# Kernel tuning notes

Hardware: AMD Instinct MI355X
Metric: run time of the kernel (lower is better)

Reference implementation:

```python
import jax, jax.numpy as jnp
import numpy as np
from jax import lax

B, C, H, W = 32, 512, 14, 14
NA = 9
N = H * W * NA  # 1764 anchors per image
IOU_THR = 0.3
SCORE_THR = 0.5
TOPK = 50


def setup_inputs() -> dict:
    key = jax.random.key(0)
    ks = jax.random.split(key, 8)
    def w(k, shape):
        return jax.random.normal(k, shape, jnp.float32) * 0.01  # nn.init.normal_(std=0.01)
    inp = {"features": jax.random.normal(ks[0], (B, C, H, W), jnp.float32)}
    # bbox head: 512->256 (GN32) ->128 (GN16) ->128 (GN16) -> 4*NA (1x1)
    inp["b1w"] = w(ks[1], (256, 512, 3, 3)); inp["b1b"] = jnp.zeros(256)
    inp["bg1w"] = jnp.ones(256); inp["bg1b"] = jnp.zeros(256)
    inp["b2w"] = w(ks[2], (128, 256, 3, 3)); inp["b2b"] = jnp.zeros(128)
    inp["bg2w"] = jnp.ones(128); inp["bg2b"] = jnp.zeros(128)
    inp["b3w"] = w(ks[3], (128, 128, 3, 3)); inp["b3b"] = jnp.zeros(128)
    inp["bg3w"] = jnp.ones(128); inp["bg3b"] = jnp.zeros(128)
    inp["b4w"] = w(ks[4], (4 * NA, 128, 1, 1)); inp["b4b"] = jnp.zeros(4 * NA)
    # classification head: 512->256 (GN32) ->128 (GN16) -> NA (1x1)
    inp["c1w"] = w(ks[5], (256, 512, 3, 3)); inp["c1b"] = jnp.zeros(256)
    inp["cg1w"] = jnp.ones(256); inp["cg1b"] = jnp.zeros(256)
    inp["c2w"] = w(ks[6], (128, 256, 3, 3)); inp["c2b"] = jnp.zeros(128)
    inp["cg2w"] = jnp.ones(128); inp["cg2b"] = jnp.zeros(128)
    inp["c3w"] = w(ks[7], (NA, 128, 1, 1)); inp["c3b"] = jnp.zeros(NA)
    return inp


def conv(x, w, b):
    k = w.shape[-1]
    pad = ((k // 2, k // 2), (k // 2, k // 2))
    y = lax.conv_general_dilated(x, w, (1, 1), pad, dimension_numbers=("NCHW", "OIHW", "NCHW"))
    return y + b[None, :, None, None]


def group_norm(x, w, b, groups, eps=1e-5):
    Bn, Cn, Hn, Wn = x.shape
    xg = x.reshape(Bn, groups, Cn // groups, Hn, Wn)
    mu = xg.mean(axis=(2, 3, 4), keepdims=True)
    var = xg.var(axis=(2, 3, 4), keepdims=True)
    xg = (xg - mu) * lax.rsqrt(var + eps)
    return xg.reshape(Bn, Cn, Hn, Wn) * w[None, :, None, None] + b[None, :, None, None]


def gelu(x):
    return jax.nn.gelu(x, approximate=False)  # torch nn.GELU default (erf)


def nms_single(boxes, scores):
    # boxes [N,4], scores [N]; greedy NMS, fixed-shape padded output [TOPK,5]
    valid = scores > SCORE_THR
    boxes = jnp.clip(boxes, 0.0, 1.0)
    order = jnp.argsort(-jnp.where(valid, scores, -jnp.inf))  # desc, invalid last
    b = boxes[order]; s = scores[order]; v = valid[order]
    x1 = jnp.maximum(b[:, None, 0], b[None, :, 0])
    y1 = jnp.maximum(b[:, None, 1], b[None, :, 1])
    x2 = jnp.minimum(b[:, None, 2], b[None, :, 2])
    y2 = jnp.minimum(b[:, None, 3], b[None, :, 3])
    inter = jnp.clip(x2 - x1, 0.0) * jnp.clip(y2 - y1, 0.0)
    area = (b[:, 2] - b[:, 0]) * (b[:, 3] - b[:, 1])
    iou = inter / (area[:, None] + area[None, :] - inter)
    # torch keeps when iou < thr; NaN compares False -> suppressed. Replicate exactly:
    suppress = jnp.logical_not(iou < IOU_THR)  # [N,N] bool
    idxs = jnp.arange(N)
    def body(suppressed, xs):
        row, i, vi = xs
        keep_i = vi & jnp.logical_not(suppressed[i])
        return suppressed | (keep_i & row & (idxs > i)), keep_i
    _, keep = lax.scan(body, jnp.zeros(N, bool), (suppress, idxs, v))
    kept_scores = jnp.where(keep, s, -1.0)
    topv, topi = lax.top_k(kept_scores, TOPK)  # first <=50 kept in score order
    out_boxes = jnp.where(topv[:, None] > 0.0, b[topi], 0.0)
    return jnp.concatenate([out_boxes, topv[:, None]], axis=-1)  # [TOPK, 5]; score=-1 marks pad


def _forward(features, b1w, b1b, bg1w, bg1b, b2w, b2b, bg2w, bg2b, b3w, b3b, bg3w, bg3b, b4w, b4b, c1w, c1b, cg1w, cg1b, c2w, c2b, cg2w, cg2b, c3w, c3b):
    bs = features.shape[0]
    h = group_norm(gelu(conv(features, b1w, b1b)), bg1w, bg1b, 32)
    h = group_norm(gelu(conv(h, b2w, b2b)), bg2w, bg2b, 16)
    h = group_norm(gelu(conv(h, b3w, b3b)), bg3w, bg3b, 16)
    bbox = conv(h, b4w, b4b).transpose(0, 2, 3, 1).reshape(bs, -1, 4)  # [B,N,4]
    h = group_norm(gelu(conv(features, c1w, c1b)), cg1w, cg1b, 32)
    h = group_norm(gelu(conv(h, c2w, c2b)), cg2w, cg2b, 16)
    conf = jax.nn.sigmoid(conv(h, c3w, c3b).transpose(0, 2, 3, 1).reshape(bs, -1))  # [B,N]
    return jax.vmap(nms_single)(bbox, conf)  # [B,TOPK,5]


def reference(features, b1w, b1b, bg1w, bg1b, b2w, b2b, bg2w, bg2b, b3w, b3b, bg3w, bg3b, b4w, b4b, c1w, c1b, cg1w, cg1b, c2w, c2b, cg2w, cg2b, c3w, c3b):
    return _forward(features, b1w, b1b, bg1w, bg1b, b2w, b2b, bg2w, bg2b, b3w, b3b, bg3w, bg3b, b4w, b4b, c1w, c1b, cg1w, cg1b, c2w, c2b, cg2w, cg2b, c3w, c3b)
```

## Files before the change

kernel.cpp:

```cpp
#include <hip/hip_runtime.h>
#include <hip/hip_bf16.h>
#include <math.h>

#define CHUNK 16
#define NN 1764
#define SORTN 2048

typedef float v2f __attribute__((ext_vector_type(2)));

template<int Co, int Ci>
__device__ inline void seg_pack_pk(const float* __restrict__ src, float* __restrict__ dst, int i) {
  int co = i / (Ci * 9); int rem = i - co * (Ci * 9); int ci = rem / 9; int k = rem - ci * 9;
  int p = (co >> 5) * 16 + (co & 15);
  int h = (co & 31) >> 4;
  dst[((size_t)ci * (Co >> 1) + p) * 20 + 2 * k + h] = src[i];
}
template<int Co, int CiK>
__device__ inline void seg_tr(const float* __restrict__ src, float* __restrict__ dst, int i) {
  int co = i / CiK; int cik = i - co * CiK;
  dst[cik * Co + co] = src[i];
}

__global__ void wtrans_all(
  const float* __restrict__ b1w, const float* __restrict__ c1w,
  const float* __restrict__ b2w, const float* __restrict__ c2w,
  const float* __restrict__ b3w, const float* __restrict__ b4w,
  const float* __restrict__ c3w,
  float* __restrict__ wp1b, float* __restrict__ wp1c,
  float* __restrict__ wp2b, float* __restrict__ wp2c,
  float* __restrict__ wp3b, float* __restrict__ wt4b, float* __restrict__ wt3c)
{
  int j = blockIdx.x * blockDim.x + threadIdx.x;
  if (j < 1179648) { seg_pack_pk<256, 512>(b1w, wp1b, j); return; } j -= 1179648;
  if (j < 1179648) { seg_pack_pk<256, 512>(c1w, wp1c, j); return; } j -= 1179648;
  if (j < 294912)  { seg_pack_pk<128, 256>(b2w, wp2b, j); return; } j -= 294912;
  if (j < 294912)  { seg_pack_pk<128, 256>(c2w, wp2c, j); return; } j -= 294912;
  if (j < 147456)  { seg_pack_pk<128, 128>(b3w, wp3b, j); return; } j -= 147456;
  if (j < 4608)    { seg_tr<36, 128>(b4w, wt4b, j); return; }  j -= 4608;
  if (j < 1152)    { seg_tr<9, 128>(c3w, wt3c, j); return; }
}

template<int COPT>
__global__ __launch_bounds__(256, 2) void conv3x3_part(
    const float* __restrict__ in0, const float* __restrict__ in1,
    const float* __restrict__ wt0, const float* __restrict__ wt1,
    float* __restrict__ po0, float* __restrict__ po1,
    int Cin, int Cout, int cobPerHead, int cinPerSplit, size_t sStride)
{
  constexpr int NP = COPT / 2;
  const int tid = threadIdx.x;
  const int bx  = blockIdx.x;
  const int b   = blockIdx.y;
  const int s   = blockIdx.z;
  const int head = bx / cobPerHead;
  const int cob  = bx - head * cobPerHead;
  const float* in  = head ? in1  : in0;
  const float* wt  = head ? wt1  : wt0;
  float* po        = head ? po1  : po0;
  const int co0 = cob * (16 * COPT);

  const int col = tid & 15;
  const int r   = tid >> 4;
  const bool ract = r < 14;

  __shared__ float tile[2][CHUNK][16][16];

  {
    float* tz = &tile[0][0][0][0];
    for (int i = tid; i < 2 * CHUNK * 256; i += 256) tz[i] = 0.0f;
  }
  __syncthreads();

  const int p = tid;
  const bool pa = p < 196;
  const int prow = p / 14, pcol = p - prow * 14;
  const float* inb = in + (size_t)b * Cin * 196;
  const int cb0 = (s * cinPerSplit) / CHUNK;
  const int nch = cinPerSplit / CHUNK;
  const int CoutH = Cout >> 1;

  int pidx[NP];
#pragma unroll
  for (int g = 0; g < NP; ++g) pidx[g] = ((co0 >> 5) + g) * 16 + col;

  if (pa) {
#pragma unroll
    for (int ci = 0; ci < CHUNK; ++ci)
      tile[0][ci][prow + 1][pcol + 1] = inb[(cb0 * CHUNK + ci) * 196 + p];
  }
  __syncthreads();

  v2f acc[NP][14];
#pragma unroll
  for (int g = 0; g < NP; ++g)
#pragma unroll
    for (int j = 0; j < 14; ++j) acc[g][j] = (v2f)(0.0f);

  for (int lcb = 0; lcb < nch; ++lcb) {
    const int cbg = cb0 + lcb;
    const int cur = lcb & 1;
    const bool more = (lcb + 1 < nch);
    float v[CHUNK];
    if (more && pa) {
#pragma unroll
      for (int ci = 0; ci < CHUNK; ++ci)
        v[ci] = inb[((cbg + 1) * CHUNK + ci) * 196 + p];
    }
    if (ract) {
      for (int ci = 0; ci < CHUNK; ++ci) {
        v2f w2[NP][9];
#pragma unroll
        for (int g = 0; g < NP; ++g) {
          const float4* wq = (const float4*)(wt +
              ((size_t)(cbg * CHUNK + ci) * CoutH + pidx[g]) * 20);
          float4 q0 = wq[0], q1 = wq[1], q2 = wq[2], q3 = wq[3], q4 = wq[4];
          w2[g][0] = (v2f){q0.x, q0.y}; w2[g][1] = (v2f){q0.z, q0.w};
          w2[g][2] = (v2f){q1.x, q1.y}; w2[g][3] = (v2f){q1.z, q1.w};
          w2[g][4] = (v2f){q2.x, q2.y}; w2[g][5] = (v2f){q2.z, q2.w};
          w2[g][6] = (v2f){q3.x, q3.y}; w2[g][7] = (v2f){q3.z, q3.w};
          w2[g][8] = (v2f){q4.x, q4.y};
        }
        float nb[3][16];
#pragma unroll
        for (int dr = 0; dr < 3; ++dr) {
          const float4* rp = (const float4*)(&tile[cur][ci][r + dr][0]);
          float4 a = rp[0], bq = rp[1], cq = rp[2], dq = rp[3];
          nb[dr][0]  = a.x;  nb[dr][1]  = a.y;  nb[dr][2]  = a.z;  nb[dr][3]  = a.w;
          nb[dr][4]  = bq.x; nb[dr][5]  = bq.y; nb[dr][6]  = bq.z; nb[dr][7]  = bq.w;
          nb[dr][8]  = cq.x; nb[dr][9]  = cq.y; nb[dr][10] = cq.z; nb[dr][11] = cq.w;
          nb[dr][12] = dq.x; nb[dr][13] = dq.y; nb[dr][14] = dq.z; nb[dr][15] = dq.w;
        }
#pragma unroll
        for (int ky = 0; ky < 3; ++ky)
#pragma unroll
          for (int kx = 0; kx < 3; ++kx) {
#pragma unroll
            for (int g = 0; g < NP; ++g) {
              v2f w = w2[g][ky * 3 + kx];
#pragma unroll
              for (int j = 0; j < 14; ++j) {
                float s_ = nb[ky][j + kx];
                v2f nbv = (v2f){s_, s_};
                acc[g][j] = __builtin_elementwise_fma(w, nbv, acc[g][j]);
              }
            }
          }
      }
    }
    if (more && pa) {
#pragma unroll
      for (int ci = 0; ci < CHUNK; ++ci)
        tile[1 - cur][ci][prow + 1][pcol + 1] = v[ci];
    }
    __syncthreads();
  }

  if (ract) {
#pragma unroll
    for (int g = 0; g < NP; ++g) {
      const int ocx = 32 * g + col;
      const int ocy = ocx + 16;
      float* opx = po + (size_t)s * sStride + ((size_t)b * Cout + co0 + ocx) * 196 + r * 14;
      float* opy = po + (size_t)s * sStride + ((size_t)b * Cout + co0 + ocy) * 196 + r * 14;
#pragma unroll
      for (int j = 0; j < 14; ++j) { opx[j] = acc[g][j].x; opy[j] = acc[g][j].y; }
    }
  }
}

template<int S>
__global__ __launch_bounds__(256) void combine_gn(
    const float* __restrict__ po0, const float* __restrict__ po1,
    const float* __restrict__ bs0, const float* __restrict__ bs1,
    const float* __restrict__ gw0, const float* __restrict__ gw1,
    const float* __restrict__ gb0, const float* __restrict__ gb1,
    float* __restrict__ out0, float* __restrict__ out1,
    int Cout, int cobPerHead, size_t sStride)
{
  const int tid = threadIdx.x, bx = blockIdx.x, b = blockIdx.y;
  const int head = bx / cobPerHead, cob = bx - head * cobPerHead;
  const float* po = head ? po1 : po0;
  const float* bs = head ? bs1 : bs0;
  const float* gw = head ? gw1 : gw0;
  const float* gb = head ? gb1 : gb0;
  float* out      = head ? out1 : out0;
  const int co0 = cob * 16;

  __shared__ float red[4][4];
  __shared__ float stats[4];

  const int p = tid;
  const bool pa = p < 196;
  float v[16];
  float s0 = 0.f, q0 = 0.f, s1 = 0.f, q1 = 0.f;
  if (pa) {
#pragma unroll
    for (int c = 0; c < 16; ++c) {
      const size_t base = ((size_t)b * Cout + co0 + c) * 196 + p;
      float x = bs[co0 + c];
#pragma unroll
      for (int s = 0; s < S; ++s) x += po[base + (size_t)s * sStride];
      float g = 0.5f * x * (1.0f + erff(x * 0.70710678118654752440f));
      v[c] = g;
      if (c < 8) { s0 += g; q0 += g * g; } else { s1 += g; q1 += g * g; }
    }
  }
#pragma unroll
  for (int off = 32; off > 0; off >>= 1) {
    s0 += __shfl_down(s0, off, 64); q0 += __shfl_down(q0, off, 64);
    s1 += __shfl_down(s1, off, 64); q1 += __shfl_down(q1, off, 64);
  }
  const int wave = tid >> 6, lane = tid & 63;
  if (lane == 0) { red[wave][0] = s0; red[wave][1] = q0; red[wave][2] = s1; red[wave][3] = q1; }
  __syncthreads();
  if (tid == 0) {
    float S0 = red[0][0] + red[1][0] + red[2][0] + red[3][0];
    float Q0 = red[0][1] + red[1][1] + red[2][1] + red[3][1];
    float S1 = red[0][2] + red[1][2] + red[2][2] + red[3][2];
    float Q1 = red[0][3] + red[1][3] + red[2][3] + red[3][3];
    float m0 = S0 * (1.0f / 1568.0f);
    float v0 = Q0 * (1.0f / 1568.0f) - m0 * m0;
    float m1 = S1 * (1.0f / 1568.0f);
    float v1 = Q1 * (1.0f / 1568.0f) - m1 * m1;
    stats[0] = m0; stats[1] = 1.0f / sqrtf(v0 + 1e-5f);
    stats[2] = m1; stats[3] = 1.0f / sqrtf(v1 + 1e-5f);
  }
  __syncthreads();
  if (pa) {
    float m0 = stats[0], i0 = stats[1], m1 = stats[2], i1 = stats[3];
#pragma unroll
    for (int c = 0; c < 16; ++c) {
      float m  = (c < 8) ? m0 : m1;
      float iv = (c < 8) ? i0 : i1;
      float y = (v[c] - m) * iv * gw[co0 + c] + gb[co0 + c];
      out[((size_t)b * Cout + co0 + c) * 196 + p] = y;
    }
  }
}

__global__ __launch_bounds__(256) void heads_1x1(
    const float* __restrict__ tb, const float* __restrict__ tc,
    const float* __restrict__ wtb, const float* __restrict__ wtc,
    const float* __restrict__ bb,  const float* __restrict__ bc,
    float* __restrict__ bbox, float* __restrict__ conf)
{
  const int b = blockIdx.x, og = blockIdx.y, tid = threadIdx.x;
  if (tid >= 196) return;
  const int p = tid;
  const bool isConf = (og == 4);
  const float* in = isConf ? tc : tb;
  const float* wbase = isConf ? wtc : (wtb + og * 9);
  const int wstride = isConf ? 9 : 36;
  const float* bsrc = isConf ? bc : (bb + og * 9);

  float a[9];
#pragma unroll
  for (int o = 0; o < 9; ++o) a[o] = bsrc[o];
  const float* pin = in + (size_t)b * 128 * 196 + p;
  for (int ci = 0; ci < 128; ++ci) {
    float x = pin[ci * 196];
    const float* w = wbase + ci * wstride;
#pragma unroll
    for (int o = 0; o < 9; ++o) a[o] = fmaf(w[o], x, a[o]);
  }
  if (isConf) {
    float* cf = conf + (size_t)b * NN + (size_t)p * 9;
#pragma unroll
    for (int o = 0; o < 9; ++o) cf[o] = 1.0f / (1.0f + expf(-a[o]));
  } else {
    float* bp = bbox + ((size_t)b * NN) * 4 + (size_t)p * 36 + og * 9;
#pragma unroll
    for (int o = 0; o < 9; ++o) bp[o] = a[o];
  }
}

__global__ __launch_bounds__(512) void nms_kernel(
  const float* __restrict__ bbox, const float* __restrict__ conf, float* __restrict__ out)
{
  const int b = blockIdx.x, tid = threadIdx.x;
  __shared__ unsigned long long key[SORTN];
  __shared__ float sx1[NN], sy1[NN], sx2[NN], sy2[NN], sar[NN], ssc[NN];
  __shared__ unsigned char sup[NN];
  __shared__ int sV, sMin;

  if (tid == 0) sV = 0;
  __syncthreads();
  int cntv = 0;
  const float* cf = conf + (size_t)b * NN;
  for (int i = tid; i < SORTN; i += 512) {
    unsigned long long k;
    if (i < NN) {
      float s = cf[i];
      unsigned rank = (unsigned)(NN - 1 - i);
      if (s > 0.5f) { k = (((unsigned long long)__float_as_uint(s)) << 32) | rank; cntv++; }
      else k = (unsigned long long)rank;
    } else k = 0ull;
    key[i] = k;
  }
  atomicAdd(&sV, cntv);
  __syncthreads();
  const int V = sV;

  for (int kk = 2; kk <= SORTN; kk <<= 1) {
    for (int j = kk >> 1; j > 0; j >>= 1) {
      for (int i = tid; i < SORTN; i += 512) {
        int ixj = i ^ j;
        if (ixj > i) {
          unsigned long long a = key[i], c = key[ixj];
          bool dirDesc = ((i & kk) == 0);
          if ((a < c) == dirDesc) { key[i] = c; key[ixj] = a; }
        }
      }
      __syncthreads();
    }
  }

  const float* bbb = bbox + (size_t)b * NN * 4;
  for (int i = tid; i < V; i += 512) {
    unsigned long long k = key[i];
    int idx = NN - 1 - (int)(unsigned)(k & 0xFFFFFFFFull);
    float s = __uint_as_float((unsigned)(k >> 32));
    const float* bp = bbb + (size_t)idx * 4;
    float x1 = fminf(fmaxf(bp[0], 0.0f), 1.0f);
    float y1 = fminf(fmaxf(bp[1], 0.0f), 1.0f);
    float x2 = fminf(fmaxf(bp[2], 0.0f), 1.0f);
    float y2 = fminf(fmaxf(bp[3], 0.0f), 1.0f);
    sx1[i] = x1; sy1[i] = y1; sx2[i] = x2; sy2[i] = y2;
    sar[i] = (x2 - x1) * (y2 - y1);
    ssc[i] = s;
    sup[i] = 0;
  }
  __syncthreads();

  int kept = 0, cur = 0;
  float* ob = out + (size_t)b * 50 * 5;
  while (kept < 50 && cur < V) {
    int nxt = -1;
    for (int base = cur; base < V; base += 512) {
      if (tid == 0) sMin = 0x7FFFFFFF;
      __syncthreads();
      int i = base + tid;
      if (i < V && !sup[i]) atomicMin(&sMin, i);
      __syncthreads();
      if (sMin != 0x7FFFFFFF) { nxt = sMin; break; }
    }
    if (nxt < 0) break;
    float kx1 = sx1[nxt], ky1 = sy1[nxt], kx2 = sx2[nxt], ky2 = sy2[nxt], ka = sar[nxt];
    if (tid == 0) {
      float* rr = ob + kept * 5;
      rr[0] = kx1; rr[1] = ky1; rr[2] = kx2; rr[3] = ky2; rr[4] = ssc[nxt];
    }
    kept++;
    for (int jj = nxt + 1 + tid; jj < V; jj += 512) {
      if (!sup[jj]) {
        float xx1 = fmaxf(kx1, sx1[jj]);
        float yy1 = fmaxf(ky1, sy1[jj]);
        float xx2 = fminf(kx2, sx2[jj]);
        float yy2 = fminf(ky2, sy2[jj]);
        float inter = fmaxf(xx2 - xx1, 0.0f) * fmaxf(yy2 - yy1, 0.0f);
        float iou = inter / ((ka + sar[jj]) - inter);
        if (!(iou < 0.3f)) sup[jj] = 1;
      }
    }
    cur = nxt + 1;
    __syncthreads();
  }
  for (int rr = kept + tid; rr < 50; rr += 512) {
    float* qq = ob + rr * 5;
    qq[0] = 0.0f; qq[1] = 0.0f; qq[2] = 0.0f; qq[3] = 0.0f; qq[4] = -1.0f;
  }
}

extern "C" void kernel_launch(void* const* d_in, const int* in_sizes, int n_in,
                              void* d_out, int out_size, void* d_ws, size_t ws_size,
                              hipStream_t stream)
{
  const float* features = (const float*)d_in[0];
  const float* b1w = (const float*)d_in[1];  const float* b1b = (const float*)d_in[2];
  const float* bg1w = (const float*)d_in[3]; const float* bg1b = (const float*)d_in[4];
  const float* b2w = (const float*)d_in[5];  const float* b2b = (const float*)d_in[6];
  const float* bg2w = (const float*)d_in[7]; const float* bg2b = (const float*)d_in[8];
  const float* b3w = (const float*)d_in[9];  const float* b3b = (const float*)d_in[10];
  const float* bg3w = (const float*)d_in[11]; const float* bg3b = (const float*)d_in[12];
  const float* b4w = (const float*)d_in[13]; const float* b4b = (const float*)d_in[14];
  const float* c1w = (const float*)d_in[15]; const float* c1b = (const float*)d_in[16];
  const float* cg1w = (const float*)d_in[17]; const float* cg1b = (const float*)d_in[18];
  const float* c2w = (const float*)d_in[19]; const float* c2b = (const float*)d_in[20];
  const float* cg2w = (const float*)d_in[21]; const float* cg2b = (const float*)d_in[22];
  const float* c3w = (const float*)d_in[23]; const float* c3b = (const float*)d_in[24];

  float* ws = (float*)d_ws;
  float* wp1b = ws; ws += 1310720;
  float* wp1c = ws; ws += 1310720;
  float* wp2b = ws; ws += 327680;
  float* wp2c = ws; ws += 327680;
  float* wp3b = ws; ws += 163840;
  float* wt4b = ws; ws += 4608;
  float* wt3c = ws; ws += 1152;
  float* t1b = ws; ws += 1605632;
  float* t1c = ws; ws += 1605632;
  float* t2b = ws; ws += 802816;
  float* t2c = ws; ws += 802816;
  float* P   = ws; ws += 12845056;
  float* bbox = ws; ws += 225792;
  float* conf = ws; ws += 56448;
  float* t3b = t1b;

  wtrans_all<<<12119, 256, 0, stream>>>(b1w, c1w, b2w, c2w, b3w, b4w, c3w,
                                        wp1b, wp1c, wp2b, wp2c, wp3b, wt4b, wt3c);

  {
    const size_t sStr = (size_t)32 * 256 * 196;
    conv3x3_part<4><<<dim3(8, 32, 4), 256, 0, stream>>>(
        features, features, wp1b, wp1c, P, P + 4 * sStr, 512, 256, 4, 128, sStr);
    combine_gn<4><<<dim3(32, 32), 256, 0, stream>>>(
        P, P + 4 * sStr, b1b, c1b, bg1w, cg1w, bg1b, cg1b, t1b, t1c, 256, 16, sStr);
  }
  {
    const size_t sStr = (size_t)32 * 128 * 196;
    conv3x3_part<4><<<dim3(4, 32, 8), 256, 0, stream>>>(
        t1b, t1c, wp2b, wp2c, P, P + 8 * sStr, 256, 128, 2, 32, sStr);
    combine_gn<8><<<dim3(16, 32), 256, 0, stream>>>(
        P, P + 8 * sStr, b2b, c2b, bg2w, cg2w, bg2b, cg2b, t2b, t2c, 128, 8, sStr);
  }
  {
    const size_t sStr = (size_t)32 * 128 * 196;
    conv3x3_part<2><<<dim3(4, 32, 8), 256, 0, stream>>>(
        t2b, t2b, wp3b, wp3b, P, P, 128, 128, 4, 16, sStr);
    combine_gn<8><<<dim3(8, 32), 256, 0, stream>>>(
        P, P, b3b, b3b, bg3w, bg3w, bg3b, bg3b, t3b, t3b, 128, 8, sStr);
  }

  heads_1x1<<<dim3(32, 5), 256, 0, stream>>>(t3b, t2c, wt4b, wt3c, b4b, c3b, bbox, conf);
  nms_kernel<<<32, 512, 0, stream>>>(bbox, conf, (float*)d_out);
}
```

Before: 782.8 us.

## Stage conv weights through LDS with register prefetch per half-chunk

The 3x3 conv kernel used to have every active thread read its packed weight vectors straight from global memory for each input channel. Now a subset of threads loads 8 input channels' worth of weights into a shared-memory buffer, prefetches the next half-chunk into registers, and stores them after a barrier. All threads then read weights from LDS. This is meant to cut redundant global and L2 weight traffic across the 14 row groups, at the cost of an extra barrier per half-chunk and more dynamic shared memory, which may reduce occupancy.

```diff
diff --git a/kernel.cpp b/kernel.cpp
--- a/kernel.cpp
+++ b/kernel.cpp
@@ -48,6 +48,8 @@
     int Cin, int Cout, int cobPerHead, int cinPerSplit, size_t sStride)
 {
   constexpr int NP = COPT / 2;
+  constexpr int NPP = 16 * NP;
+  constexpr int NPAIR = 8 * NPP;
   const int tid = threadIdx.x;
   const int bx  = blockIdx.x;
   const int b   = blockIdx.y;
@@ -63,11 +65,12 @@
   const int r   = tid >> 4;
   const bool ract = r < 14;
 
-  __shared__ float tile[2][CHUNK][16][16];
+  extern __shared__ float smem[];
+  float (*tile)[CHUNK][16][16] = (float(*)[CHUNK][16][16])smem;
+  float (*wlds)[NPP][20] = (float(*)[NPP][20])(smem + 2 * CHUNK * 256);
 
   {
-    float* tz = &tile[0][0][0][0];
-    for (int i = tid; i < 2 * CHUNK * 256; i += 256) tz[i] = 0.0f;
+    for (int i = tid; i < 2 * CHUNK * 256; i += 256) smem[i] = 0.0f;
   }
   __syncthreads();
 
@@ -79,14 +82,21 @@
   const int nch = cinPerSplit / CHUNK;
   const int CoutH = Cout >> 1;
 
-  int pidx[NP];
-#pragma unroll
-  for (int g = 0; g < NP; ++g) pidx[g] = ((co0 >> 5) + g) * 16 + col;
+  const int sciL = tid / NPP;
+  const int spp  = tid - sciL * NPP;
+  const bool sact = tid < NPAIR;
+  const int spidx = ((co0 >> 5) + (spp >> 4)) * 16 + (spp & 15);
 
   if (pa) {
 #pragma unroll
     for (int ci = 0; ci < CHUNK; ++ci)
       tile[0][ci][prow + 1][pcol + 1] = inb[(cb0 * CHUNK + ci) * 196 + p];
+  }
+  if (sact) {
+    const float4* src = (const float4*)(wt + ((size_t)(cb0 * CHUNK + sciL) * CoutH + spidx) * 20);
+    float4 q0 = src[0], q1 = src[1], q2 = src[2], q3 = src[3], q4 = src[4];
+    float4* dst = (float4*)&wlds[sciL][spp][0];
+    dst[0] = q0; dst[1] = q1; dst[2] = q2; dst[3] = q3; dst[4] = q4;
   }
   __syncthreads();
 
@@ -106,53 +116,69 @@
       for (int ci = 0; ci < CHUNK; ++ci)
         v[ci] = inb[((cbg + 1) * CHUNK + ci) * 196 + p];
     }
-    if (ract) {
-      for (int ci = 0; ci < CHUNK; ++ci) {
-        v2f w2[NP][9];
-#pragma unroll
-        for (int g = 0; g < NP; ++g) {
-          const float4* wq = (const float4*)(wt +
-              ((size_t)(cbg * CHUNK + ci) * CoutH + pidx[g]) * 20);
-          float4 q0 = wq[0], q1 = wq[1], q2 = wq[2], q3 = wq[3], q4 = wq[4];
-          w2[g][0] = (v2f){q0.x, q0.y}; w2[g][1] = (v2f){q0.z, q0.w};
-          w2[g][2] = (v2f){q1.x, q1.y}; w2[g][3] = (v2f){q1.z, q1.w};
-          w2[g][4] = (v2f){q2.x, q2.y}; w2[g][5] = (v2f){q2.z, q2.w};
-          w2[g][6] = (v2f){q3.x, q3.y}; w2[g][7] = (v2f){q3.z, q3.w};
-          w2[g][8] = (v2f){q4.x, q4.y};
-        }
-        float nb[3][16];
-#pragma unroll
-        for (int dr = 0; dr < 3; ++dr) {
-          const float4* rp = (const float4*)(&tile[cur][ci][r + dr][0]);
-          float4 a = rp[0], bq = rp[1], cq = rp[2], dq = rp[3];
-          nb[dr][0]  = a.x;  nb[dr][1]  = a.y;  nb[dr][2]  = a.z;  nb[dr][3]  = a.w;
-          nb[dr][4]  = bq.x; nb[dr][5]  = bq.y; nb[dr][6]  = bq.z; nb[dr][7]  = bq.w;
-          nb[dr][8]  = cq.x; nb[dr][9]  = cq.y; nb[dr][10] = cq.z; nb[dr][11] = cq.w;
-          nb[dr][12] = dq.x; nb[dr][13] = dq.y; nb[dr][14] = dq.z; nb[dr][15] = dq.w;
-        }
-#pragma unroll
-        for (int ky = 0; ky < 3; ++ky)
-#pragma unroll
-          for (int kx = 0; kx < 3; ++kx) {
-#pragma unroll
-            for (int g = 0; g < NP; ++g) {
-              v2f w = w2[g][ky * 3 + kx];
-#pragma unroll
-              for (int j = 0; j < 14; ++j) {
-                float s_ = nb[ky][j + kx];
-                v2f nbv = (v2f){s_, s_};
-                acc[g][j] = __builtin_elementwise_fma(w, nbv, acc[g][j]);
+#pragma unroll
+    for (int half = 0; half < 2; ++half) {
+      const bool hasNext = (half == 0) || more;
+      const int nbase = (half == 0) ? (cbg * CHUNK + 8) : ((cbg + 1) * CHUNK);
+      float4 q0, q1, q2, q3, q4;
+      if (hasNext && sact) {
+        const float4* src = (const float4*)(wt + ((size_t)(nbase + sciL) * CoutH + spidx) * 20);
+        q0 = src[0]; q1 = src[1]; q2 = src[2]; q3 = src[3]; q4 = src[4];
+      }
+      if (ract) {
+#pragma unroll
+        for (int ciL = 0; ciL < 8; ++ciL) {
+          const int ci = half * 8 + ciL;
+          v2f w2[NP][9];
+#pragma unroll
+          for (int g = 0; g < NP; ++g) {
+            const float4* wq = (const float4*)&wlds[ciL][g * 16 + col][0];
+            float4 a0 = wq[0], a1 = wq[1], a2 = wq[2], a3 = wq[3], a4 = wq[4];
+            w2[g][0] = (v2f){a0.x, a0.y}; w2[g][1] = (v2f){a0.z, a0.w};
+            w2[g][2] = (v2f){a1.x, a1.y}; w2[g][3] = (v2f){a1.z, a1.w};
+            w2[g][4] = (v2f){a2.x, a2.y}; w2[g][5] = (v2f){a2.z, a2.w};
+            w2[g][6] = (v2f){a3.x, a3.y}; w2[g][7] = (v2f){a3.z, a3.w};
+            w2[g][8] = (v2f){a4.x, a4.y};
+          }
+          float nb[3][16];
+#pragma unroll
+          for (int dr = 0; dr < 3; ++dr) {
+            const float4* rp = (const float4*)(&tile[cur][ci][r + dr][0]);
+            float4 a = rp[0], bq = rp[1], cq = rp[2], dq = rp[3];
+            nb[dr][0]  = a.x;  nb[dr][1]  = a.y;  nb[dr][2]  = a.z;  nb[dr][3]  = a.w;
+            nb[dr][4]  = bq.x; nb[dr][5]  = bq.y; nb[dr][6]  = bq.z; nb[dr][7]  = bq.w;
+            nb[dr][8]  = cq.x; nb[dr][9]  = cq.y; nb[dr][10] = cq.z; nb[dr][11] = cq.w;
+            nb[dr][12] = dq.x; nb[dr][13] = dq.y; nb[dr][14] = dq.z; nb[dr][15] = dq.w;
+          }
+#pragma unroll
+          for (int ky = 0; ky < 3; ++ky)
+#pragma unroll
+            for (int kx = 0; kx < 3; ++kx) {
+#pragma unroll
+              for (int g = 0; g < NP; ++g) {
+                v2f w = w2[g][ky * 3 + kx];
+#pragma unroll
+                for (int j = 0; j < 14; ++j) {
+                  float s_ = nb[ky][j + kx];
+                  v2f nbv = (v2f){s_, s_};
+                  acc[g][j] = __builtin_elementwise_fma(w, nbv, acc[g][j]);
+                }
               }
             }
-          }
-      }
-    }
-    if (more && pa) {
-#pragma unroll
-      for (int ci = 0; ci < CHUNK; ++ci)
-        tile[1 - cur][ci][prow + 1][pcol + 1] = v[ci];
-    }
-    __syncthreads();
+        }
+      }
+      __syncthreads();
+      if (hasNext && sact) {
+        float4* dst = (float4*)&wlds[sciL][spp][0];
+        dst[0] = q0; dst[1] = q1; dst[2] = q2; dst[3] = q3; dst[4] = q4;
+      }
+      if (half == 1 && more && pa) {
+#pragma unroll
+        for (int ci = 0; ci < CHUNK; ++ci)
+          tile[1 - cur][ci][prow + 1][pcol + 1] = v[ci];
+      }
+      __syncthreads();
+    }
   }
 
   if (ract) {
@@ -409,23 +435,26 @@
   wtrans_all<<<12119, 256, 0, stream>>>(b1w, c1w, b2w, c2w, b3w, b4w, c3w,
                                         wp1b, wp1c, wp2b, wp2c, wp3b, wt4b, wt3c);
 
+  const size_t lds4 = (size_t)(2 * CHUNK * 256 + 8 * 32 * 20) * 4;
+  const size_t lds2 = (size_t)(2 * CHUNK * 256 + 8 * 16 * 20) * 4;
+
   {
     const size_t sStr = (size_t)32 * 256 * 196;
-    conv3x3_part<4><<<dim3(8, 32, 4), 256, 0, stream>>>(
+    conv3x3_part<4><<<dim3(8, 32, 4), 256, lds4, stream>>>(
         features, features, wp1b, wp1c, P, P + 4 * sStr, 512, 256, 4, 128, sStr);
     combine_gn<4><<<dim3(32, 32), 256, 0, stream>>>(
         P, P + 4 * sStr, b1b, c1b, bg1w, cg1w, bg1b, cg1b, t1b, t1c, 256, 16, sStr);
   }
   {
     const size_t sStr = (size_t)32 * 128 * 196;
-    conv3x3_part<4><<<dim3(4, 32, 8), 256, 0, stream>>>(
+    conv3x3_part<4><<<dim3(4, 32, 8), 256, lds4, stream>>>(
         t1b, t1c, wp2b, wp2c, P, P + 8 * sStr, 256, 128, 2, 32, sStr);
     combine_gn<8><<<dim3(16, 32), 256, 0, stream>>>(
         P, P + 8 * sStr, b2b, c2b, bg2w, cg2w, bg2b, cg2b, t2b, t2c, 128, 8, sStr);
   }
   {
     const size_t sStr = (size_t)32 * 128 * 196;
-    conv3x3_part<2><<<dim3(4, 32, 8), 256, 0, stream>>>(
+    conv3x3_part<2><<<dim3(4, 32, 8), 256, lds2, stream>>>(
         t2b, t2b, wp3b, wp3b, P, P, 128, 128, 4, 16, sStr);
     combine_gn<8><<<dim3(8, 32), 256, 0, stream>>>(
         P, P, b3b, b3b, bg3w, bg3w, bg3b, bg3b, t3b, t3b, 128, 8, sStr);
```

After: 745.3 us. 1.05x faster.
